# Optimization experiments

Hardware: AMD Instinct MI355X
Metric: run time of the kernel (lower is better)

The kernel has to match this reference:

```python
import jax, jax.numpy as jnp
import numpy as np

N = 100000      # nodes
E = 3200000     # edges (avg degree 32)
F_IN = 256      # n_features
HID = 128       # n_hidden
C = 16          # n_classes
K = 10          # propagation hops


def setup_inputs() -> dict:
    key = jax.random.key(0)
    ks = jax.random.split(key, 12)
    x = jax.random.normal(ks[0], (N, F_IN), jnp.float32)
    edge_index = jax.random.randint(ks[1], (2, E), 0, N, dtype=jnp.int64)
    edge_attr = jax.random.uniform(ks[2], (E,), jnp.float32)
    # learned parameters (torch Linear layout: W [out, in], b [out])
    def lin(k, fan_out, fan_in):
        s = 1.0 / np.sqrt(fan_in)
        kw, kb = jax.random.split(k)
        W = jax.random.uniform(kw, (fan_out, fan_in), jnp.float32, -s, s)
        b = jax.random.uniform(kb, (fan_out,), jnp.float32, -s, s)
        return W, b
    lin1_w, lin1_b = lin(ks[3], HID, F_IN)
    lin2_w, lin2_b = lin(ks[4], HID, HID)   # hidden lin (n_layers-3 == 1)
    lin3_w, lin3_b = lin(ks[5], C, HID)     # classes lin
    proj_w, proj_b = lin(ks[6], 1, C)       # Prop retain-score projection
    return {"x": x, "edge_index": edge_index, "edge_attr": edge_attr,
            "lin1_w": lin1_w, "lin1_b": lin1_b,
            "lin2_w": lin2_w, "lin2_b": lin2_b,
            "lin3_w": lin3_w, "lin3_b": lin3_b,
            "proj_w": proj_w, "proj_b": proj_b}


def reference(x, edge_index, edge_attr,
              lin1_w, lin1_b, lin2_w, lin2_b, lin3_w, lin3_b,
              proj_w, proj_b):
    # MLP stack (dropout is identity in eval mode)
    h = jax.nn.relu(x @ lin1_w.T + lin1_b)
    h = jax.nn.relu(h @ lin2_w.T + lin2_b)
    h = jax.nn.relu(h @ lin3_w.T + lin3_b)          # [N, C]

    src, dst = edge_index[0], edge_index[1]
    norm = edge_attr[:, None]                        # [E, 1]

    def hop(carry, _):
        msg = norm * carry[src]                      # gather + scale [E, C]
        nxt = jax.ops.segment_sum(msg, dst, num_segments=N)  # scatter-add
        return nxt, nxt

    _, hops = jax.lax.scan(hop, h, None, length=K)   # [K, N, C]
    pps = jnp.concatenate([h[None], hops], axis=0)   # [K+1, N, C]
    pps = jnp.transpose(pps, (1, 0, 2))              # [N, K+1, C]

    # adaptive combination: sigmoid(Linear(C->1)) per hop, weighted sum
    score = jax.nn.sigmoid(jnp.einsum('nkc,c->nk', pps, proj_w[0]) + proj_b[0])
    out = jnp.einsum('nk,nkc->nc', score, pps)       # [N, C]
    return out
```

## Files before the change

kernel.cpp:

```cpp
#include <hip/hip_runtime.h>
#include <hip/hip_bf16.h>
#include <math.h>

#define N_NODES 100000
#define E_EDGES 3200000
#define K_HOPS  10
#define NPP     256
#define NPART   ((N_NODES + NPP - 1) / NPP)
#define CHUNK   4096
#define EPT     (CHUNK / 256)
#define NCHUNK  ((E_EDGES + CHUNK - 1) / CHUNK)
#define NFLAT   (NPART * NCHUNK)
#define SSEG    8192
#define GA      ((NFLAT + SSEG - 1) / SSEG)

typedef __attribute__((ext_vector_type(8))) short short8;
typedef __attribute__((ext_vector_type(4))) float floatx4;

__device__ __forceinline__ ushort f2bf(float f) {
    uint u = __float_as_uint(f);
    u += 0x7fffu + ((u >> 16) & 1u);
    return (ushort)(u >> 16);
}
__device__ __forceinline__ uint pk2(float a, float b) {
    return (uint)f2bf(a) | ((uint)f2bf(b) << 16);
}
__device__ __forceinline__ float bflo(uint u) { return __uint_as_float(u << 16); }
__device__ __forceinline__ float bfhi(uint u) { return __uint_as_float(u & 0xffff0000u); }

template<int KD, int MD, bool A_F32>
__global__ __launch_bounds__(256) void mfma_mlp(
    const void* __restrict__ Av, const float* __restrict__ W,
    const float* __restrict__ bias, ushort* __restrict__ C)
{
    constexpr int NCT = MD / 16;
    constexpr int LDW = 88;
    __shared__ ushort Wl[MD * LDW];

    const int t    = threadIdx.x;
    const int w    = t >> 6;
    const int lane = t & 63;
    const int m    = lane & 15;
    const int quad = lane >> 4;
    const int rowBase = blockIdx.x * 128 + w * 32;

    floatx4 acc[2][NCT];
#pragma unroll
    for (int rt = 0; rt < 2; ++rt)
#pragma unroll
        for (int ct = 0; ct < NCT; ++ct) acc[rt][ct] = (floatx4)0.f;

    for (int kb = 0; kb < KD; kb += 64) {
#pragma unroll
        for (int j = 0; j < MD / 16; ++j) {
            int flat = j * 256 + t;
            int n  = flat >> 4;
            int c4 = (flat & 15) * 4;
            floatx4 v = *(const floatx4*)&W[(size_t)n * KD + kb + c4];
            *(uint2*)&Wl[n * LDW + c4] = make_uint2(pk2(v[0], v[1]), pk2(v[2], v[3]));
        }
        __syncthreads();
#pragma unroll
        for (int ks = 0; ks < 64; ks += 32) {
            short8 af[2];
#pragma unroll
            for (int rt = 0; rt < 2; ++rt) {
                int row = rowBase + rt * 16 + m;
                row = row < N_NODES ? row : N_NODES - 1;
                size_t base = (size_t)row * KD + kb + ks + quad * 8;
                if constexpr (A_F32) {
                    const float* ap = (const float*)Av + base;
                    floatx4 a0 = *(const floatx4*)ap;
                    floatx4 a1 = *(const floatx4*)(ap + 4);
                    short8 x;
                    x[0] = (short)f2bf(a0[0]); x[1] = (short)f2bf(a0[1]);
                    x[2] = (short)f2bf(a0[2]); x[3] = (short)f2bf(a0[3]);
                    x[4] = (short)f2bf(a1[0]); x[5] = (short)f2bf(a1[1]);
                    x[6] = (short)f2bf(a1[2]); x[7] = (short)f2bf(a1[3]);
                    af[rt] = x;
                } else {
                    af[rt] = *(const short8*)((const ushort*)Av + base);
                }
            }
#pragma unroll
            for (int ct = 0; ct < NCT; ++ct) {
                short8 bf = *(const short8*)&Wl[(ct * 16 + m) * LDW + ks + quad * 8];
#pragma unroll
                for (int rt = 0; rt < 2; ++rt)
                    acc[rt][ct] = __builtin_amdgcn_mfma_f32_16x16x32_bf16(
                        af[rt], bf, acc[rt][ct], 0, 0, 0);
            }
        }
        __syncthreads();
    }

#pragma unroll
    for (int rt = 0; rt < 2; ++rt) {
#pragma unroll
        for (int r = 0; r < 4; ++r) {
            int row = rowBase + rt * 16 + quad * 4 + r;
            if (row < N_NODES) {
#pragma unroll
                for (int ct = 0; ct < NCT; ++ct) {
                    int col = ct * 16 + m;
                    float v = acc[rt][ct][r] + bias[col];
                    v = v > 0.f ? v : 0.f;
                    C[(size_t)row * MD + col] = f2bf(v);
                }
            }
        }
    }
}

__global__ __launch_bounds__(256) void hist2(
    const int* __restrict__ dst, int* __restrict__ cmat)
{
    __shared__ int lhist[NPART];
    const int t = threadIdx.x;
    for (int p = t; p < NPART; p += 256) lhist[p] = 0;
    __syncthreads();
    const int base = blockIdx.x * CHUNK;
#pragma unroll
    for (int j = 0; j < EPT; ++j) {
        int i = base + j * 256 + t;
        if (i < E_EDGES) atomicAdd(&lhist[dst[i] >> 8], 1);
    }
    __syncthreads();
    for (int p = t; p < NPART; p += 256)
        cmat[p * NCHUNK + blockIdx.x] = lhist[p];
}

__global__ __launch_bounds__(1024) void scan_reduce(
    const int* __restrict__ cmat, int* __restrict__ bsum)
{
    __shared__ int wsum[16];
    const int t = threadIdx.x, lane = t & 63, wid = t >> 6;
    int base = blockIdx.x * SSEG + t * 8;
    int s = 0;
#pragma unroll
    for (int j = 0; j < 8; ++j) {
        int idx = base + j;
        if (idx < NFLAT) s += cmat[idx];
    }
#pragma unroll
    for (int d = 1; d < 64; d <<= 1) s += __shfl_xor(s, d);
    if (lane == 0) wsum[wid] = s;
    __syncthreads();
    if (t == 0) {
        int tot = 0;
#pragma unroll
        for (int i = 0; i < 16; ++i) tot += wsum[i];
        bsum[blockIdx.x] = tot;
    }
}

__global__ void scan_tops(const int* __restrict__ bsum, int* __restrict__ boff)
{
    const int t = threadIdx.x;
    int v = (t < GA) ? bsum[t] : 0;
    int x = v;
#pragma unroll
    for (int d = 1; d < 64; d <<= 1) {
        int y = __shfl_up(x, d);
        if (t >= d) x += y;
    }
    if (t < GA) boff[t] = x - v;
}

__global__ __launch_bounds__(1024) void scan_apply(
    int* __restrict__ cmat, const int* __restrict__ boff, int* __restrict__ pbase)
{
    __shared__ int wsum[16];
    __shared__ int woff[17];
    const int t = threadIdx.x, lane = t & 63, wid = t >> 6;
    int base = blockIdx.x * SSEG + t * 8;
    int v[8], pre[8];
    int s = 0;
#pragma unroll
    for (int j = 0; j < 8; ++j) {
        int idx = base + j;
        v[j] = (idx < NFLAT) ? cmat[idx] : 0;
        pre[j] = s;
        s += v[j];
    }
    int x = s;
#pragma unroll
    for (int d = 1; d < 64; d <<= 1) {
        int y = __shfl_up(x, d);
        if (lane >= d) x += y;
    }
    if (lane == 63) wsum[wid] = x;
    __syncthreads();
    if (wid == 0) {
        int w = (lane < 16) ? wsum[lane] : 0;
#pragma unroll
        for (int d = 1; d < 16; d <<= 1) {
            int y = __shfl_up(w, d);
            if (lane >= d) w += y;
        }
        if (lane < 16) woff[lane + 1] = w;
        if (lane == 0) woff[0] = 0;
    }
    __syncthreads();
    int tbase = boff[blockIdx.x] + woff[wid] + (x - s);
#pragma unroll
    for (int j = 0; j < 8; ++j) {
        int idx = base + j;
        if (idx < NFLAT) {
            int e = tbase + pre[j];
            cmat[idx] = e;
            if (idx % NCHUNK == 0) pbase[idx / NCHUNK] = e;
        }
    }
    if (blockIdx.x == 0 && t == 0) pbase[NPART] = E_EDGES;
}

__global__ __launch_bounds__(256) void scatter3(
    const int* __restrict__ src, const int* __restrict__ dst,
    const float* __restrict__ ea, const int* __restrict__ cbase,
    int2* __restrict__ staging)
{
    __shared__ int2 ebuf[CHUNK];
    __shared__ int  gaddr[CHUNK];
    __shared__ int  lcnt[NPART];
    __shared__ int  goff[NPART];
    __shared__ int  wsum[4];
    const int t = threadIdx.x;
    const int b = blockIdx.x;
    const int base = b * CHUNK;
    const int cnt = min(CHUNK, E_EDGES - base);
    const int lane = t & 63, wid = t >> 6;

    for (int p = t; p < NPART; p += 256) lcnt[p] = 0;
    __syncthreads();

    int d[EPT];
#pragma unroll
    for (int j = 0; j < EPT; ++j) {
        int i = base + j * 256 + t;
        d[j] = (i < E_EDGES) ? dst[i] : -1;
        if (d[j] >= 0) atomicAdd(&lcnt[d[j] >> 8], 1);
    }
    __syncthreads();

    int v0 = (2 * t     < NPART) ? lcnt[2 * t]     : 0;
    int v1 = (2 * t + 1 < NPART) ? lcnt[2 * t + 1] : 0;
    int pair = v0 + v1;
    int x = pair;
#pragma unroll
    for (int dd = 1; dd < 64; dd <<= 1) {
        int y = __shfl_up(x, dd);
        if (lane >= dd) x += y;
    }
    if (lane == 63) wsum[wid] = x;
    __syncthreads();
    int wbase = 0;
#pragma unroll
    for (int w = 0; w < 4; ++w) if (w < wid) wbase += wsum[w];
    int excl = wbase + x - pair;
    if (2 * t < NPART) {
        lcnt[2 * t] = excl;
        goff[2 * t] = cbase[(2 * t) * NCHUNK + b] - excl;
    }
    if (2 * t + 1 < NPART) {
        lcnt[2 * t + 1] = excl + v0;
        goff[2 * t + 1] = cbase[(2 * t + 1) * NCHUNK + b] - (excl + v0);
    }
    __syncthreads();

#pragma unroll
    for (int j = 0; j < EPT; ++j) {
        if (d[j] >= 0) {
            int i = base + j * 256 + t;
            int p = d[j] >> 8;
            int s = atomicAdd(&lcnt[p], 1);
            ebuf[s]  = make_int2(__float_as_int(ea[i]),
                                 src[i] | ((d[j] & 255) << 17));
            gaddr[s] = goff[p] + s;
        }
    }
    __syncthreads();

    for (int k = t; k < cnt; k += 256)
        staging[gaddr[k]] = ebuf[k];
}

__global__ __launch_bounds__(1024) void partition_build(
    const int2* __restrict__ staging, const int* __restrict__ pbase,
    int* __restrict__ rowp, int2* __restrict__ csr)
{
    __shared__ int ncnt[NPP];
    __shared__ int wsum[4];
    const int p = blockIdx.x;
    const int t = threadIdx.x;
    const int e0 = pbase[p], e1 = pbase[p + 1];
    const int cnt = e1 - e0;
    const int n0 = p << 8;

    if (t < NPP) ncnt[t] = 0;
    __syncthreads();
    for (int e = t; e < cnt; e += 1024)
        atomicAdd(&ncnt[(staging[e0 + e].y >> 17) & 255], 1);
    __syncthreads();

    int x = 0, v = 0;
    if (t < NPP) {
        const int lane = t & 63, wid = t >> 6;
        v = ncnt[t];
        x = v;
#pragma unroll
        for (int d = 1; d < 64; d <<= 1) {
            int y = __shfl_up(x, d);
            if (lane >= d) x += y;
        }
        if (lane == 63) wsum[wid] = x;
    }
    __syncthreads();
    if (t < NPP) {
        const int wid = t >> 6;
        int wbase = 0;
#pragma unroll
        for (int w = 0; w < 4; ++w) if (w < wid) wbase += wsum[w];
        int excl = wbase + x - v;
        ncnt[t] = e0 + excl;
        int n = n0 + t;
        if (n < N_NODES) rowp[n] = e0 + excl;
    }
    if (p == NPART - 1 && t == 0) rowp[N_NODES] = E_EDGES;
    __syncthreads();

    for (int e = t; e < cnt; e += 1024) {
        int2 en = staging[e0 + e];
        int dlo = (en.y >> 17) & 255;
        int pos = atomicAdd(&ncnt[dlo], 1);
        csr[pos] = make_int2(en.y & 0x1FFFF, en.x);
    }
}

__global__ __launch_bounds__(256) void init_out_bf16(
    const ushort* __restrict__ h, const float* __restrict__ pw,
    const float* __restrict__ pb, float* __restrict__ out)
{
    const int t = threadIdx.x;
    const int l = t & 1;
    const int n = blockIdx.x * 128 + (t >> 1);
    if (n >= N_NODES) return;
    uint4 v = *(const uint4*)&h[(size_t)n * 16 + l * 8];
    float a0 = bflo(v.x), a1 = bfhi(v.x), a2 = bflo(v.y), a3 = bfhi(v.y);
    float a4 = bflo(v.z), a5 = bfhi(v.z), a6 = bflo(v.w), a7 = bfhi(v.w);
    float4 p0 = ((const float4*)pw)[l * 2];
    float4 p1 = ((const float4*)pw)[l * 2 + 1];
    float part = a0 * p0.x + a1 * p0.y + a2 * p0.z + a3 * p0.w
               + a4 * p1.x + a5 * p1.y + a6 * p1.z + a7 * p1.w;
    part += __shfl_xor(part, 1);
    float s = 1.f / (1.f + __expf(-(part + pb[0])));
    *(float4*)&out[(size_t)n * 16 + l * 8]     = make_float4(s*a0, s*a1, s*a2, s*a3);
    *(float4*)&out[(size_t)n * 16 + l * 8 + 4] = make_float4(s*a4, s*a5, s*a6, s*a7);
}

__global__ __launch_bounds__(256) void hop_bf16(
    const ushort* __restrict__ prev, ushort* __restrict__ next,
    const int* __restrict__ rowp, const int2* __restrict__ csr,
    const float* __restrict__ pw, const float* __restrict__ pb,
    float* __restrict__ out)
{
    const int t = threadIdx.x;
    const int l = t & 1;
    const int g = (t >> 1) & 3;
    const int n = blockIdx.x * 32 + (t >> 3);
    if (n >= N_NODES) return;
    const int e0 = rowp[n], e1 = rowp[n + 1];
    float a[8];
#pragma unroll
    for (int j = 0; j < 8; ++j) a[j] = 0.f;

    int e = e0 + g;
    for (; e + 12 < e1; e += 16) {
        int2 c0 = csr[e];
        int2 c1 = csr[e + 4];
        int2 c2 = csr[e + 8];
        int2 c3 = csr[e + 12];
        float w0 = __int_as_float(c0.y), w1 = __int_as_float(c1.y);
        float w2 = __int_as_float(c2.y), w3 = __int_as_float(c3.y);
        uint4 v0 = *(const uint4*)&prev[(size_t)c0.x * 16 + l * 8];
        uint4 v1 = *(const uint4*)&prev[(size_t)c1.x * 16 + l * 8];
        uint4 v2 = *(const uint4*)&prev[(size_t)c2.x * 16 + l * 8];
        uint4 v3 = *(const uint4*)&prev[(size_t)c3.x * 16 + l * 8];
        a[0] += w0 * bflo(v0.x); a[1] += w0 * bfhi(v0.x);
        a[2] += w0 * bflo(v0.y); a[3] += w0 * bfhi(v0.y);
        a[4] += w0 * bflo(v0.z); a[5] += w0 * bfhi(v0.z);
        a[6] += w0 * bflo(v0.w); a[7] += w0 * bfhi(v0.w);
        a[0] += w1 * bflo(v1.x); a[1] += w1 * bfhi(v1.x);
        a[2] += w1 * bflo(v1.y); a[3] += w1 * bfhi(v1.y);
        a[4] += w1 * bflo(v1.z); a[5] += w1 * bfhi(v1.z);
        a[6] += w1 * bflo(v1.w); a[7] += w1 * bfhi(v1.w);
        a[0] += w2 * bflo(v2.x); a[1] += w2 * bfhi(v2.x);
        a[2] += w2 * bflo(v2.y); a[3] += w2 * bfhi(v2.y);
        a[4] += w2 * bflo(v2.z); a[5] += w2 * bfhi(v2.z);
        a[6] += w2 * bflo(v2.w); a[7] += w2 * bfhi(v2.w);
        a[0] += w3 * bflo(v3.x); a[1] += w3 * bfhi(v3.x);
        a[2] += w3 * bflo(v3.y); a[3] += w3 * bfhi(v3.y);
        a[4] += w3 * bflo(v3.z); a[5] += w3 * bfhi(v3.z);
        a[6] += w3 * bflo(v3.w); a[7] += w3 * bfhi(v3.w);
    }
    for (; e < e1; e += 4) {
        int2 c0 = csr[e];
        float w0 = __int_as_float(c0.y);
        uint4 v0 = *(const uint4*)&prev[(size_t)c0.x * 16 + l * 8];
        a[0] += w0 * bflo(v0.x); a[1] += w0 * bfhi(v0.x);
        a[2] += w0 * bflo(v0.y); a[3] += w0 * bfhi(v0.y);
        a[4] += w0 * bflo(v0.z); a[5] += w0 * bfhi(v0.z);
        a[6] += w0 * bflo(v0.w); a[7] += w0 * bfhi(v0.w);
    }

#pragma unroll
    for (int d = 2; d <= 4; d <<= 1) {
#pragma unroll
        for (int j = 0; j < 8; ++j) a[j] += __shfl_xor(a[j], d);
    }

    float4 p0 = ((const float4*)pw)[l * 2];
    float4 p1 = ((const float4*)pw)[l * 2 + 1];
    float part = a[0]*p0.x + a[1]*p0.y + a[2]*p0.z + a[3]*p0.w
               + a[4]*p1.x + a[5]*p1.y + a[6]*p1.z + a[7]*p1.w;
    part += __shfl_xor(part, 1);
    float s = 1.f / (1.f + __expf(-(part + pb[0])));

    if (g == 0) {
        uint4 nv = make_uint4(pk2(a[0], a[1]), pk2(a[2], a[3]),
                              pk2(a[4], a[5]), pk2(a[6], a[7]));
        *(uint4*)&next[(size_t)n * 16 + l * 8] = nv;
        float4 o0 = *(float4*)&out[(size_t)n * 16 + l * 8];
        float4 o1 = *(float4*)&out[(size_t)n * 16 + l * 8 + 4];
        o0.x += s*a[0]; o0.y += s*a[1]; o0.z += s*a[2]; o0.w += s*a[3];
        o1.x += s*a[4]; o1.y += s*a[5]; o1.z += s*a[6]; o1.w += s*a[7];
        *(float4*)&out[(size_t)n * 16 + l * 8]     = o0;
        *(float4*)&out[(size_t)n * 16 + l * 8 + 4] = o1;
    }
}

extern "C" void kernel_launch(void* const* d_in, const int* in_sizes, int n_in,
                              void* d_out, int out_size, void* d_ws, size_t ws_size,
                              hipStream_t stream)
{
    const float* x  = (const float*)d_in[0];
    const int*   ei = (const int*)d_in[1];
    const float* ea = (const float*)d_in[2];
    const float* w1 = (const float*)d_in[3];
    const float* b1 = (const float*)d_in[4];
    const float* w2 = (const float*)d_in[5];
    const float* b2 = (const float*)d_in[6];
    const float* w3 = (const float*)d_in[7];
    const float* b3 = (const float*)d_in[8];
    const float* pw = (const float*)d_in[9];
    const float* pb = (const float*)d_in[10];
    float* out = (float*)d_out;

    char* ws = (char*)d_ws;
    size_t off = 0;
    char*   region0 = ws + off;           off += (size_t)E_EDGES * 16;
    ushort* pingb = (ushort*)(ws + off);  off += (size_t)N_NODES * 16 * 2;
    ushort* pongb = (ushort*)(ws + off);  off += (size_t)N_NODES * 16 * 2;
    int*    rowp  = (int*)(ws + off);     off += (((size_t)(N_NODES + 1) * 4) + 15) & ~(size_t)15;
    int*    cmat  = (int*)(ws + off);     off += ((size_t)NFLAT * 4 + 15) & ~(size_t)15;
    int*    bsum  = (int*)(ws + off);     off += ((size_t)GA * 4 + 15) & ~(size_t)15;
    int*    boff  = (int*)(ws + off);     off += ((size_t)GA * 4 + 15) & ~(size_t)15;
    int*    pbase = (int*)(ws + off);     off += ((size_t)(NPART + 1) * 4 + 15) & ~(size_t)15;
    int2*   csr   = (int2*)(ws + off);    off += (size_t)E_EDGES * 8;

    int2*   staging = (int2*)region0;
    ushort* h1b = (ushort*)region0;
    ushort* h2b = (ushort*)(region0 + (size_t)N_NODES * 128 * 2);

    const int* src = ei;
    const int* dst = ei + E_EDGES;

    const dim3 blk(256);
    const int mlpGrid    = (N_NODES + 127) / 128;
    const int hopGrid    = (N_NODES + 31) / 32;

    hist2<<<NCHUNK, blk, 0, stream>>>(dst, cmat);
    scan_reduce<<<GA, 1024, 0, stream>>>(cmat, bsum);
    scan_tops<<<1, 64, 0, stream>>>(bsum, boff);
    scan_apply<<<GA, 1024, 0, stream>>>(cmat, boff, pbase);
    scatter3<<<NCHUNK, blk, 0, stream>>>(src, dst, ea, cmat, staging);
    partition_build<<<NPART, 1024, 0, stream>>>(staging, pbase, rowp, csr);

    mfma_mlp<256, 128, true ><<<mlpGrid, blk, 0, stream>>>(x,   w1, b1, h1b);
    mfma_mlp<128, 128, false><<<mlpGrid, blk, 0, stream>>>(h1b, w2, b2, h2b);
    mfma_mlp<128,  16, false><<<mlpGrid, blk, 0, stream>>>(h2b, w3, b3, pingb);

    init_out_bf16<<<mlpGrid, blk, 0, stream>>>(pingb, pw, pb, out);

    const ushort* prev = pingb;
    ushort* next = pongb;
    for (int k = 0; k < K_HOPS; ++k) {
        hop_bf16<<<hopGrid, blk, 0, stream>>>(prev, next, rowp, csr, pw, pb, out);
        ushort* tmp = (ushort*)prev; prev = next; next = tmp;
    }
}
```

Baseline: 602.3 us.

## Fuse three MLP layers and output init into one LDS-resident kernel

Replaces three separate MFMA GEMM launches plus the init_out kernel with a single fused kernel. Intermediate hidden activations stay in shared memory, with an XOR-swizzled layout, instead of round-tripping through global memory. The per-hop sigmoid score initialization is computed in the last layer's epilogue. This removes roughly 100 MB of intermediate global traffic and three launches. In exchange it uses more LDS and registers per block (the input fragments are preloaded), which may lower occupancy.

```diff
diff --git a/kernel.cpp b/kernel.cpp
--- a/kernel.cpp
+++ b/kernel.cpp
@@ -28,14 +28,17 @@
 __device__ __forceinline__ float bflo(uint u) { return __uint_as_float(u << 16); }
 __device__ __forceinline__ float bfhi(uint u) { return __uint_as_float(u & 0xffff0000u); }
 
-template<int KD, int MD, bool A_F32>
-__global__ __launch_bounds__(256) void mfma_mlp(
-    const void* __restrict__ Av, const float* __restrict__ W,
-    const float* __restrict__ bias, ushort* __restrict__ C)
-{
-    constexpr int NCT = MD / 16;
-    constexpr int LDW = 88;
-    __shared__ ushort Wl[MD * LDW];
+__global__ __launch_bounds__(256, 3) void fused_mlp(
+    const float* __restrict__ X,
+    const float* __restrict__ W1, const float* __restrict__ B1,
+    const float* __restrict__ W2, const float* __restrict__ B2,
+    const float* __restrict__ W3, const float* __restrict__ B3,
+    const float* __restrict__ PW, const float* __restrict__ PB,
+    ushort* __restrict__ H0,
+    float* __restrict__ OUT)
+{
+    __shared__ ushort Wl[128 * 64];
+    __shared__ ushort Hb[128 * 128];
 
     const int t    = threadIdx.x;
     const int w    = t >> 6;
@@ -43,73 +46,185 @@
     const int m    = lane & 15;
     const int quad = lane >> 4;
     const int rowBase = blockIdx.x * 128 + w * 32;
-
-    floatx4 acc[2][NCT];
+    const int swm = (m & 7) << 3;
+
+    short8 afr[2][8];
+#pragma unroll
+    for (int rt = 0; rt < 2; ++rt) {
+        int row = rowBase + rt * 16 + m;
+        row = row < N_NODES ? row : N_NODES - 1;
+        const float* xp = X + (size_t)row * 256 + quad * 8;
+#pragma unroll
+        for (int kk = 0; kk < 8; ++kk) {
+            floatx4 a0 = *(const floatx4*)(xp + kk * 32);
+            floatx4 a1 = *(const floatx4*)(xp + kk * 32 + 4);
+            short8 v;
+            v[0] = (short)f2bf(a0[0]); v[1] = (short)f2bf(a0[1]);
+            v[2] = (short)f2bf(a0[2]); v[3] = (short)f2bf(a0[3]);
+            v[4] = (short)f2bf(a1[0]); v[5] = (short)f2bf(a1[1]);
+            v[6] = (short)f2bf(a1[2]); v[7] = (short)f2bf(a1[3]);
+            afr[rt][kk] = v;
+        }
+    }
+
+    floatx4 acc[2][8];
 #pragma unroll
     for (int rt = 0; rt < 2; ++rt)
 #pragma unroll
-        for (int ct = 0; ct < NCT; ++ct) acc[rt][ct] = (floatx4)0.f;
-
-    for (int kb = 0; kb < KD; kb += 64) {
-#pragma unroll
-        for (int j = 0; j < MD / 16; ++j) {
+        for (int ct = 0; ct < 8; ++ct) acc[rt][ct] = (floatx4)0.f;
+
+#pragma unroll 1
+    for (int kb4 = 0; kb4 < 4; ++kb4) {
+#pragma unroll
+        for (int j = 0; j < 8; ++j) {
             int flat = j * 256 + t;
             int n  = flat >> 4;
             int c4 = (flat & 15) * 4;
-            floatx4 v = *(const floatx4*)&W[(size_t)n * KD + kb + c4];
-            *(uint2*)&Wl[n * LDW + c4] = make_uint2(pk2(v[0], v[1]), pk2(v[2], v[3]));
+            floatx4 v = *(const floatx4*)&W1[(size_t)n * 256 + kb4 * 64 + c4];
+            *(uint2*)&Wl[n * 64 + (c4 ^ ((n & 7) << 3))] =
+                make_uint2(pk2(v[0], v[1]), pk2(v[2], v[3]));
         }
         __syncthreads();
 #pragma unroll
-        for (int ks = 0; ks < 64; ks += 32) {
-            short8 af[2];
-#pragma unroll
-            for (int rt = 0; rt < 2; ++rt) {
-                int row = rowBase + rt * 16 + m;
-                row = row < N_NODES ? row : N_NODES - 1;
-                size_t base = (size_t)row * KD + kb + ks + quad * 8;
-                if constexpr (A_F32) {
-                    const float* ap = (const float*)Av + base;
-                    floatx4 a0 = *(const floatx4*)ap;
-                    floatx4 a1 = *(const floatx4*)(ap + 4);
-                    short8 x;
-                    x[0] = (short)f2bf(a0[0]); x[1] = (short)f2bf(a0[1]);
-                    x[2] = (short)f2bf(a0[2]); x[3] = (short)f2bf(a0[3]);
-                    x[4] = (short)f2bf(a1[0]); x[5] = (short)f2bf(a1[1]);
-                    x[6] = (short)f2bf(a1[2]); x[7] = (short)f2bf(a1[3]);
-                    af[rt] = x;
-                } else {
-                    af[rt] = *(const short8*)((const ushort*)Av + base);
+        for (int ks = 0; ks < 2; ++ks) {
+            int kk = kb4 * 2 + ks;
+#pragma unroll
+            for (int ct = 0; ct < 8; ++ct) {
+                short8 bf = *(const short8*)
+                    &Wl[(ct * 16 + m) * 64 + ((ks * 32 + quad * 8) ^ swm)];
+                acc[0][ct] = __builtin_amdgcn_mfma_f32_16x16x32_bf16(
+                    afr[0][kk], bf, acc[0][ct], 0, 0, 0);
+                acc[1][ct] = __builtin_amdgcn_mfma_f32_16x16x32_bf16(
+                    afr[1][kk], bf, acc[1][ct], 0, 0, 0);
+            }
+        }
+        __syncthreads();
+    }
+
+    {
+        float br[8];
+#pragma unroll
+        for (int ct = 0; ct < 8; ++ct) br[ct] = B1[ct * 16 + m];
+#pragma unroll
+        for (int rt = 0; rt < 2; ++rt)
+#pragma unroll
+            for (int r = 0; r < 4; ++r) {
+                int lrow = w * 32 + rt * 16 + quad * 4 + r;
+                int sw = (lrow & 7) << 3;
+#pragma unroll
+                for (int ct = 0; ct < 8; ++ct) {
+                    float v = acc[rt][ct][r] + br[ct];
+                    v = v > 0.f ? v : 0.f;
+                    Hb[lrow * 128 + ((ct * 16 + m) ^ sw)] = f2bf(v);
                 }
             }
-#pragma unroll
-            for (int ct = 0; ct < NCT; ++ct) {
-                short8 bf = *(const short8*)&Wl[(ct * 16 + m) * LDW + ks + quad * 8];
-#pragma unroll
-                for (int rt = 0; rt < 2; ++rt)
-                    acc[rt][ct] = __builtin_amdgcn_mfma_f32_16x16x32_bf16(
-                        af[rt], bf, acc[rt][ct], 0, 0, 0);
+    }
+
+#pragma unroll
+    for (int rt = 0; rt < 2; ++rt)
+#pragma unroll
+        for (int ct = 0; ct < 8; ++ct) acc[rt][ct] = (floatx4)0.f;
+
+#pragma unroll 1
+    for (int kb2 = 0; kb2 < 2; ++kb2) {
+#pragma unroll
+        for (int j = 0; j < 8; ++j) {
+            int flat = j * 256 + t;
+            int n  = flat >> 4;
+            int c4 = (flat & 15) * 4;
+            floatx4 v = *(const floatx4*)&W2[(size_t)n * 128 + kb2 * 64 + c4];
+            *(uint2*)&Wl[n * 64 + (c4 ^ ((n & 7) << 3))] =
+                make_uint2(pk2(v[0], v[1]), pk2(v[2], v[3]));
+        }
+        __syncthreads();
+#pragma unroll
+        for (int ks = 0; ks < 2; ++ks) {
+            short8 af[2];
+#pragma unroll
+            for (int rt = 0; rt < 2; ++rt) {
+                int lrow = w * 32 + rt * 16 + m;
+                int col  = kb2 * 64 + ks * 32 + quad * 8;
+                af[rt] = *(const short8*)&Hb[lrow * 128 + (col ^ swm)];
             }
+#pragma unroll
+            for (int ct = 0; ct < 8; ++ct) {
+                short8 bf = *(const short8*)
+                    &Wl[(ct * 16 + m) * 64 + ((ks * 32 + quad * 8) ^ swm)];
+                acc[0][ct] = __builtin_amdgcn_mfma_f32_16x16x32_bf16(
+                    af[0], bf, acc[0][ct], 0, 0, 0);
+                acc[1][ct] = __builtin_amdgcn_mfma_f32_16x16x32_bf16(
+                    af[1], bf, acc[1][ct], 0, 0, 0);
+            }
         }
         __syncthreads();
     }
 
-#pragma unroll
-    for (int rt = 0; rt < 2; ++rt) {
+    {
+        float br[8];
+#pragma unroll
+        for (int ct = 0; ct < 8; ++ct) br[ct] = B2[ct * 16 + m];
+#pragma unroll
+        for (int rt = 0; rt < 2; ++rt)
+#pragma unroll
+            for (int r = 0; r < 4; ++r) {
+                int lrow = w * 32 + rt * 16 + quad * 4 + r;
+                int sw = (lrow & 7) << 3;
+#pragma unroll
+                for (int ct = 0; ct < 8; ++ct) {
+                    float v = acc[rt][ct][r] + br[ct];
+                    v = v > 0.f ? v : 0.f;
+                    Hb[lrow * 128 + ((ct * 16 + m) ^ sw)] = f2bf(v);
+                }
+            }
+    }
+
+#pragma unroll
+    for (int j = 0; j < 2; ++j) {
+        int flat = j * 256 + t;
+        int n  = flat >> 5;
+        int c4 = (flat & 31) * 4;
+        floatx4 v = *(const floatx4*)&W3[(size_t)n * 128 + c4];
+        *(uint2*)&Wl[n * 128 + (c4 ^ ((n & 7) << 3))] =
+            make_uint2(pk2(v[0], v[1]), pk2(v[2], v[3]));
+    }
+    __syncthreads();
+
+    floatx4 acc3[2];
+    acc3[0] = (floatx4)0.f; acc3[1] = (floatx4)0.f;
+#pragma unroll
+    for (int ks4 = 0; ks4 < 4; ++ks4) {
+        int col = ks4 * 32 + quad * 8;
+        short8 bf = *(const short8*)&Wl[m * 128 + (col ^ swm)];
+#pragma unroll
+        for (int rt = 0; rt < 2; ++rt) {
+            int lrow = w * 32 + rt * 16 + m;
+            short8 af = *(const short8*)&Hb[lrow * 128 + (col ^ swm)];
+            acc3[rt] = __builtin_amdgcn_mfma_f32_16x16x32_bf16(
+                af, bf, acc3[rt], 0, 0, 0);
+        }
+    }
+
+    const float pwm = PW[m];
+    const float b3m = B3[m];
+    const float pb0 = PB[0];
+#pragma unroll
+    for (int rt = 0; rt < 2; ++rt)
 #pragma unroll
         for (int r = 0; r < 4; ++r) {
             int row = rowBase + rt * 16 + quad * 4 + r;
+            float v = acc3[rt][r] + b3m;
+            v = v > 0.f ? v : 0.f;
+            float part = v * pwm;
+            part += __shfl_xor(part, 1);
+            part += __shfl_xor(part, 2);
+            part += __shfl_xor(part, 4);
+            part += __shfl_xor(part, 8);
+            float s = 1.f / (1.f + __expf(-(part + pb0)));
             if (row < N_NODES) {
-#pragma unroll
-                for (int ct = 0; ct < NCT; ++ct) {
-                    int col = ct * 16 + m;
-                    float v = acc[rt][ct][r] + bias[col];
-                    v = v > 0.f ? v : 0.f;
-                    C[(size_t)row * MD + col] = f2bf(v);
-                }
+                OUT[(size_t)row * 16 + m] = s * v;
+                H0[(size_t)row * 16 + m]  = f2bf(v);
             }
         }
-    }
 }
 
 __global__ __launch_bounds__(256) void hist2(
@@ -335,27 +450,6 @@
         int pos = atomicAdd(&ncnt[dlo], 1);
         csr[pos] = make_int2(en.y & 0x1FFFF, en.x);
     }
-}
-
-__global__ __launch_bounds__(256) void init_out_bf16(
-    const ushort* __restrict__ h, const float* __restrict__ pw,
-    const float* __restrict__ pb, float* __restrict__ out)
-{
-    const int t = threadIdx.x;
-    const int l = t & 1;
-    const int n = blockIdx.x * 128 + (t >> 1);
-    if (n >= N_NODES) return;
-    uint4 v = *(const uint4*)&h[(size_t)n * 16 + l * 8];
-    float a0 = bflo(v.x), a1 = bfhi(v.x), a2 = bflo(v.y), a3 = bfhi(v.y);
-    float a4 = bflo(v.z), a5 = bfhi(v.z), a6 = bflo(v.w), a7 = bfhi(v.w);
-    float4 p0 = ((const float4*)pw)[l * 2];
-    float4 p1 = ((const float4*)pw)[l * 2 + 1];
-    float part = a0 * p0.x + a1 * p0.y + a2 * p0.z + a3 * p0.w
-               + a4 * p1.x + a5 * p1.y + a6 * p1.z + a7 * p1.w;
-    part += __shfl_xor(part, 1);
-    float s = 1.f / (1.f + __expf(-(part + pb[0])));
-    *(float4*)&out[(size_t)n * 16 + l * 8]     = make_float4(s*a0, s*a1, s*a2, s*a3);
-    *(float4*)&out[(size_t)n * 16 + l * 8 + 4] = make_float4(s*a4, s*a5, s*a6, s*a7);
 }
 
 __global__ __launch_bounds__(256) void hop_bf16(
@@ -469,8 +563,6 @@
     int2*   csr   = (int2*)(ws + off);    off += (size_t)E_EDGES * 8;
 
     int2*   staging = (int2*)region0;
-    ushort* h1b = (ushort*)region0;
-    ushort* h2b = (ushort*)(region0 + (size_t)N_NODES * 128 * 2);
 
     const int* src = ei;
     const int* dst = ei + E_EDGES;
@@ -486,11 +578,8 @@
     scatter3<<<NCHUNK, blk, 0, stream>>>(src, dst, ea, cmat, staging);
     partition_build<<<NPART, 1024, 0, stream>>>(staging, pbase, rowp, csr);
 
-    mfma_mlp<256, 128, true ><<<mlpGrid, blk, 0, stream>>>(x,   w1, b1, h1b);
-    mfma_mlp<128, 128, false><<<mlpGrid, blk, 0, stream>>>(h1b, w2, b2, h2b);
-    mfma_mlp<128,  16, false><<<mlpGrid, blk, 0, stream>>>(h2b, w3, b3, pingb);
-
-    init_out_bf16<<<mlpGrid, blk, 0, stream>>>(pingb, pw, pb, out);
+    fused_mlp<<<mlpGrid, blk, 0, stream>>>(x, w1, b1, w2, b2, w3, b3,
+                                           pw, pb, pingb, out);
 
     const ushort* prev = pingb;
     ushort* next = pongb;
```

After: 621.7 us. 3.2% more time.
